# Optimization experiments

Measured on AMD Instinct MI355X. Metric: run time of the kernel, lower is better.

The kernel has to match this reference:

```python
import jax, jax.numpy as jnp
import numpy as np

N = 8192          # tokens
D_IN = 32768      # dec_input_size (SAE latent dim)
D_OUT = 768       # dec_hidden_size (model resid dim)


def setup_inputs() -> dict:
    key = jax.random.key(0)
    kx, kw = jax.random.split(key)
    x = jax.random.normal(kx, (N, D_IN), dtype=jnp.float32)
    W = jax.random.normal(kw, (D_OUT, D_IN), dtype=jnp.float32) * (1.0 / np.sqrt(D_IN))
    b_pre = jnp.zeros((D_IN,), dtype=jnp.float32)
    return {"x": x, "W": W, "b_pre": b_pre}


def reference(x, W, b_pre):
    # x: [N, D_in]; subtract pre-bias, then dense decode: (x - b_pre) @ W^T -> [N, D_out]
    x_adj = x - b_pre
    return jnp.einsum('nd,od->no', x_adj, W)
```

## Files before the change

### kernel.cpp

```cpp
#include <hip/hip_runtime.h>
#include <hip/hip_bf16.h>

#define TOK 8192
#define OUTD 768
#define KD 32768

#define BM 128
#define BN 768
#define BK 32
#define SPLITK 4
#define KCHUNK (KD / SPLITK)
#define NKT (KCHUNK / BK)
#define NHT_TOT (KD / BK)
#define THREADS 512
#define HTILE (BN * BK * 2)
#define ATILE (BM * BK * 2)

typedef __attribute__((ext_vector_type(4))) float f32x4;
typedef __attribute__((ext_vector_type(16))) float f32x16;
typedef __attribute__((ext_vector_type(8))) short bf16x8;
typedef __attribute__((ext_vector_type(4))) unsigned int u32x4;

__device__ __forceinline__ unsigned pack2(float lo, float hi) {
    __hip_bfloat162 h = __float22bfloat162_rn(make_float2(lo, hi));
    unsigned u;
    __builtin_memcpy(&u, &h, 4);
    return u;
}

__device__ __forceinline__ u32x4 cvt_chunk(f32x4 a, f32x4 b) {
    u32x4 r;
    r[0] = pack2(a[0], a[1]);
    r[1] = pack2(a[2], a[3]);
    r[2] = pack2(b[0], b[1]);
    r[3] = pack2(b[2], b[3]);
    return r;
}

__global__ void colbias_kernel(const float* __restrict__ W,
                               const float* __restrict__ bp,
                               float* __restrict__ negc) {
    int o = blockIdx.x;
    int tid = threadIdx.x;
    const float* wr = W + (long)o * KD;
    float s = 0.f;
    for (int i = tid * 4; i < KD; i += 256 * 4) {
        f32x4 w = *(const f32x4*)(wr + i);
        f32x4 b = *(const f32x4*)(bp + i);
        s += w[0] * b[0] + w[1] * b[1] + w[2] * b[2] + w[3] * b[3];
    }
    #pragma unroll
    for (int off = 32; off > 0; off >>= 1) s += __shfl_down(s, off);
    __shared__ float red[4];
    if ((tid & 63) == 0) red[tid >> 6] = s;
    __syncthreads();
    if (tid == 0) negc[o] = -(red[0] + red[1] + red[2] + red[3]);
}

__global__ void init_kernel(const float* __restrict__ negc,
                            float* __restrict__ out) {
    long idx = ((long)blockIdx.x * blockDim.x + threadIdx.x) * 4;
    int col = (int)(idx % OUTD);
    f32x4 v = *(const f32x4*)(negc + col);
    *(f32x4*)(out + idx) = v;
}

__global__ void cast_w_kernel(const float* __restrict__ W,
                              char* __restrict__ wsW) {
    int kth = blockIdx.x;
    int tid = threadIdx.x;
    int q = tid & 3;
    int c0 = tid >> 2;
    #pragma unroll
    for (int i = 0; i < 6; ++i) {
        int c = c0 + i * 128;
        const float* src = W + (long)c * KD + kth * 32 + q * 8;
        f32x4 a = ((const f32x4*)src)[0];
        f32x4 b = ((const f32x4*)src)[1];
        char* dst = wsW + (long)kth * HTILE + c * 64 + ((q ^ (c & 3)) << 4);
        *(u32x4*)dst = cvt_chunk(a, b);
    }
}

__global__ __launch_bounds__(THREADS, 2) void decoder_gemm(
    const float* __restrict__ X, const char* __restrict__ Wb16,
    float* __restrict__ Out) {
    __shared__ char lds[2 * ATILE + 2 * HTILE];
    char* ldsA = lds;
    char* ldsB = lds + 2 * ATILE;

    const int bid = blockIdx.x;
    const int ks = bid & (SPLITK - 1);
    const int mt = bid >> 2;
    const int row0 = mt * BM;

    const int tid = threadIdx.x;
    const int lane = tid & 63;
    const int wid = tid >> 6;
    const int wm = wid >> 2;
    const int wn = wid & 3;
    const int l31 = lane & 31;
    const int hi = lane >> 5;

    const float* Xb = X + (long)row0 * KD + (long)ks * KCHUNK;
    const char* Wt0 = Wb16 + (long)ks * NKT * HTILE;

    const int ar = tid >> 2;
    const int aq = tid & 3;
    f32x4 xr[2];

    auto LOADA = [&](int kt) {
        const f32x4* p = (const f32x4*)(Xb + (long)ar * KD + kt * 32 + aq * 8);
        xr[0] = p[0];
        xr[1] = p[1];
    };

    const int asoff = ar * 64 + ((aq ^ (ar & 3)) << 4);

    auto STOREA = [&](int buf) {
        *(u32x4*)(ldsA + buf * ATILE + asoff) = cvt_chunk(xr[0], xr[1]);
    };

    auto ISSUEB = [&](int kt, int buf) {
        const char* src = Wt0 + (long)kt * HTILE + tid * 16;
        char* dst = ldsB + buf * HTILE + tid * 16;
        #pragma unroll
        for (int j = 0; j < 6; ++j)
            __builtin_amdgcn_global_load_lds(
                (const __attribute__((address_space(1))) void*)(src + j * 8192),
                (__attribute__((address_space(3))) void*)(dst + j * 8192),
                16, 0, 0);
    };

    int aoff[2], boff[6];
    #pragma unroll
    for (int m = 0; m < 2; ++m) {
        int row = wm * 64 + m * 32 + l31;
        aoff[m] = row * 64 + ((hi ^ (row & 3)) << 4);
    }
    #pragma unroll
    for (int n = 0; n < 6; ++n) {
        int col = wn * 192 + n * 32 + l31;
        boff[n] = col * 64 + ((hi ^ (col & 3)) << 4);
    }

    f32x16 acc[2][6];
    #pragma unroll
    for (int m = 0; m < 2; ++m)
        #pragma unroll
        for (int n = 0; n < 6; ++n)
            #pragma unroll
            for (int r = 0; r < 16; ++r) acc[m][n][r] = 0.f;

    ISSUEB(0, 0);
    LOADA(0);
    STOREA(0);
    __syncthreads();

    for (int kt = 0; kt < NKT; ++kt) {
        const int cur = kt & 1;
        const bool more = (kt + 1 < NKT);
        if (more) {
            ISSUEB(kt + 1, cur ^ 1);
            LOADA(kt + 1);
        }

        const char* As = ldsA + cur * ATILE;
        const char* Bs = ldsB + cur * HTILE;
        #pragma unroll
        for (int kk = 0; kk < 2; ++kk) {
            bf16x8 afr[2], bfr[6];
            #pragma unroll
            for (int m = 0; m < 2; ++m)
                afr[m] = *(const bf16x8*)(As + (aoff[m] ^ (kk << 5)));
            #pragma unroll
            for (int n = 0; n < 6; ++n)
                bfr[n] = *(const bf16x8*)(Bs + (boff[n] ^ (kk << 5)));
            __builtin_amdgcn_s_setprio(1);
            #pragma unroll
            for (int m = 0; m < 2; ++m)
                #pragma unroll
                for (int n = 0; n < 6; ++n)
                    acc[m][n] = __builtin_amdgcn_mfma_f32_32x32x16_bf16(
                        afr[m], bfr[n], acc[m][n], 0, 0, 0);
            __builtin_amdgcn_s_setprio(0);
        }

        if (more) STOREA(cur ^ 1);
        __syncthreads();
    }

    #pragma unroll
    for (int m = 0; m < 2; ++m) {
        int rowb = row0 + wm * 64 + m * 32 + 4 * hi;
        #pragma unroll
        for (int n = 0; n < 6; ++n) {
            int col = wn * 192 + n * 32 + l31;
            #pragma unroll
            for (int r = 0; r < 16; ++r) {
                int row = rowb + (r & 3) + 8 * (r >> 2);
                atomicAdd(&Out[(long)row * OUTD + col], acc[m][n][r]);
            }
        }
    }
}

extern "C" void kernel_launch(void* const* d_in, const int* in_sizes, int n_in,
                              void* d_out, int out_size, void* d_ws,
                              size_t ws_size, hipStream_t stream) {
    const float* x = (const float*)d_in[0];
    const float* W = (const float*)d_in[1];
    const float* bp = (const float*)d_in[2];
    float* out = (float*)d_out;
    float* negc = (float*)d_ws;
    char* wsW = (char*)d_ws + 4096;

    hipLaunchKernelGGL(colbias_kernel, dim3(OUTD), dim3(256), 0, stream, W, bp,
                       negc);
    hipLaunchKernelGGL(init_kernel, dim3((TOK * OUTD) / (256 * 4)), dim3(256),
                       0, stream, negc, out);
    hipLaunchKernelGGL(cast_w_kernel, dim3(NHT_TOT), dim3(512), 0, stream, W,
                       wsW);
    hipLaunchKernelGGL(decoder_gemm, dim3((TOK / BM) * SPLITK), dim3(THREADS),
                       0, stream, x, wsW, out);
}
```

Baseline: 596.3 us.

## Change LDS swizzle and restructure main loop with explicit waitcnt barriers

Changes the XOR swizzle for the A and B LDS tiles to use bits 1-2 of the row index instead of bits 0-1, which alters the LDS bank-conflict pattern for the MFMA fragment reads. It also replaces the double-buffered loop's __syncthreads with hand-placed s_waitcnt vmcnt/lgkmcnt plus raw s_barrier and sched_barriers. The B prefetch for the next tile is now issued after the barrier, and the A global load is overlapped more explicitly with compute. The aim is to cut barrier and wait overhead in the k-loop. The risk is that correctness depends on the vmcnt(2) count matching the number of outstanding loads.

```diff
diff --git a/kernel.cpp b/kernel.cpp
--- a/kernel.cpp
+++ b/kernel.cpp
@@ -77,7 +77,8 @@
         const float* src = W + (long)c * KD + kth * 32 + q * 8;
         f32x4 a = ((const f32x4*)src)[0];
         f32x4 b = ((const f32x4*)src)[1];
-        char* dst = wsW + (long)kth * HTILE + c * 64 + ((q ^ (c & 3)) << 4);
+        char* dst = wsW + (long)kth * HTILE + c * 64 +
+                    ((q ^ ((c >> 1) & 3)) << 4);
         *(u32x4*)dst = cvt_chunk(a, b);
     }
 }
@@ -115,7 +116,7 @@
         xr[1] = p[1];
     };
 
-    const int asoff = ar * 64 + ((aq ^ (ar & 3)) << 4);
+    const int asoff = ar * 64 + ((aq ^ ((ar >> 1) & 3)) << 4);
 
     auto STOREA = [&](int buf) {
         *(u32x4*)(ldsA + buf * ATILE + asoff) = cvt_chunk(xr[0], xr[1]);
@@ -136,12 +137,12 @@
     #pragma unroll
     for (int m = 0; m < 2; ++m) {
         int row = wm * 64 + m * 32 + l31;
-        aoff[m] = row * 64 + ((hi ^ (row & 3)) << 4);
+        aoff[m] = row * 64 + ((hi ^ ((row >> 1) & 3)) << 4);
     }
     #pragma unroll
     for (int n = 0; n < 6; ++n) {
         int col = wn * 192 + n * 32 + l31;
-        boff[n] = col * 64 + ((hi ^ (col & 3)) << 4);
+        boff[n] = col * 64 + ((hi ^ ((col >> 1) & 3)) << 4);
     }
 
     f32x16 acc[2][6];
@@ -152,19 +153,7 @@
             #pragma unroll
             for (int r = 0; r < 16; ++r) acc[m][n][r] = 0.f;
 
-    ISSUEB(0, 0);
-    LOADA(0);
-    STOREA(0);
-    __syncthreads();
-
-    for (int kt = 0; kt < NKT; ++kt) {
-        const int cur = kt & 1;
-        const bool more = (kt + 1 < NKT);
-        if (more) {
-            ISSUEB(kt + 1, cur ^ 1);
-            LOADA(kt + 1);
-        }
-
+    auto COMPUTE = [&](int cur) {
         const char* As = ldsA + cur * ATILE;
         const char* Bs = ldsB + cur * HTILE;
         #pragma unroll
@@ -185,10 +174,31 @@
                         afr[m], bfr[n], acc[m][n], 0, 0, 0);
             __builtin_amdgcn_s_setprio(0);
         }
-
-        if (more) STOREA(cur ^ 1);
-        __syncthreads();
-    }
+    };
+
+    LOADA(0);
+    ISSUEB(0, 0);
+    STOREA(0);
+    asm volatile("s_waitcnt lgkmcnt(0)" ::: "memory");
+
+    for (int kt = 0; kt < NKT - 1; ++kt) {
+        const int cur = kt & 1;
+        LOADA(kt + 1);
+        asm volatile("s_waitcnt vmcnt(2)" ::: "memory");
+        __builtin_amdgcn_sched_barrier(0);
+        __builtin_amdgcn_s_barrier();
+        __builtin_amdgcn_sched_barrier(0);
+        ISSUEB(kt + 1, cur ^ 1);
+        COMPUTE(cur);
+        STOREA(cur ^ 1);
+        asm volatile("s_waitcnt lgkmcnt(0)" ::: "memory");
+    }
+
+    asm volatile("s_waitcnt vmcnt(0)" ::: "memory");
+    __builtin_amdgcn_sched_barrier(0);
+    __builtin_amdgcn_s_barrier();
+    __builtin_amdgcn_sched_barrier(0);
+    COMPUTE((NKT - 1) & 1);
 
     #pragma unroll
     for (int m = 0; m < 2; ++m) {
```

Result: slower. 661.0 us (+10.8%).
